# Kernel tuning notes

Hardware: AMD Instinct MI355X
Metric: run time of the kernel (lower is better)

## Reference

```python
import jax, jax.numpy as jnp
import numpy as np

T = 16384  # sequence length (scan axis)
D = 512    # d_model


def setup_inputs() -> dict:
    key = jax.random.key(0)
    k1, k2, k3, k4 = jax.random.split(key, 4)
    inputs = jax.random.normal(k1, (T, D), dtype=jnp.float32)
    terminations = jax.random.bernoulli(k2, 0.01, (T,))
    c0 = jnp.zeros((D,), dtype=jnp.float32)
    h0 = jnp.zeros((D,), dtype=jnp.float32)
    # flax OptimizedLSTMCell fuses the 4 gates (order i, f, g, o) into one kernel
    scale = 1.0 / np.sqrt(D).astype(np.float32)
    Wx = jax.random.normal(k3, (D, 4 * D), dtype=jnp.float32) * scale  # input kernel (no bias in flax)
    Wh = jax.random.normal(k4, (D, 4 * D), dtype=jnp.float32) * scale  # recurrent kernel
    b = jnp.zeros((4 * D,), dtype=jnp.float32)                          # recurrent-dense bias
    return {"inputs": inputs, "terminations": terminations, "c0": c0, "h0": h0,
            "Wx": Wx, "Wh": Wh, "b": b}


def reference(inputs, terminations, c0, h0, Wx, Wh, b):
    def step(carry, xt):
        x, term = xt
        c, h = carry
        # reset_on_terminate: zero the carry when this step begins a new episode
        keep = jnp.where(term, jnp.zeros((), c.dtype), jnp.ones((), c.dtype))
        c = c * keep
        h = h * keep
        # fused gate pre-activations, flax gate order: i, f, g, o
        z = x @ Wx + h @ Wh + b  # [4*D]
        i, f, g, o = jnp.split(z, 4, axis=-1)
        new_c = jax.nn.sigmoid(f) * c + jax.nn.sigmoid(i) * jnp.tanh(g)
        new_h = jax.nn.sigmoid(o) * jnp.tanh(new_c)
        return (new_c, new_h), (new_c, new_h)

    _, (cs, hs) = jax.lax.scan(step, (c0, h0), (inputs, terminations))
    # original returns (y_t, new_states) with y_t == new_h per step -> (hs, (cs, hs))
    return hs, cs, hs
```

## Files before the change

### kernel.cpp

```cpp
#include <hip/hip_runtime.h>

typedef _Float16 half8 __attribute__((ext_vector_type(8)));
typedef float floatx4 __attribute__((ext_vector_type(4)));
typedef unsigned int u32x4 __attribute__((ext_vector_type(4)));
typedef unsigned long long u64;
typedef unsigned int u32;
typedef unsigned short u16;

#define T_LEN 16384
#define DM 512
#define NC 2048
#define NG 16
#define NR 16
#define WPG 16
#define WVG 32

struct Meta { int S; int use_h0; int steps_g[NG]; };

union FragU { u64 q[2]; u32x4 r; half8 v; };

__device__ __forceinline__ float sigf(float x) { return 1.0f / (1.0f + __expf(-x)); }
__device__ __forceinline__ float tanh_f(float x) { return 1.0f - 2.0f / (__expf(2.0f * x) + 1.0f); }

__global__ void zero_kernel(u32* __restrict__ p, size_t nwords) {
    size_t i = (size_t)blockIdx.x * blockDim.x + threadIdx.x;
    size_t stride = (size_t)gridDim.x * blockDim.x;
    for (; i < nwords; i += stride) p[i] = 0u;
}

__global__ void pack_f16_kernel(const float* __restrict__ src, _Float16* __restrict__ dst, int n8) {
    int i = blockIdx.x * blockDim.x + threadIdx.x;
    if (i >= n8) return;
    const floatx4* s = (const floatx4*)src + (size_t)i * 2;
    floatx4 a = s[0], b = s[1];
    half8 o;
    o[0] = (_Float16)a[0]; o[1] = (_Float16)a[1]; o[2] = (_Float16)a[2]; o[3] = (_Float16)a[3];
    o[4] = (_Float16)b[0]; o[5] = (_Float16)b[1]; o[6] = (_Float16)b[2]; o[7] = (_Float16)b[3];
    ((half8*)dst)[i] = o;
}

__global__ __launch_bounds__(256) void pack_w_kernel(const float* __restrict__ src, half8* __restrict__ dst) {
    int wid = blockIdx.x * 4 + (threadIdx.x >> 6);
    int l = threadIdx.x & 63;
    int tt = wid >> 4, kt = wid & 15;
    int q = tt & 3, cch = tt >> 2;
    int col = q * 512 + cch * 16 + (l & 15);
    int h = l >> 4;
    half8 o;
#pragma unroll
    for (int jj = 0; jj < 8; jj++) o[jj] = (_Float16)src[(size_t)(kt * 32 + h * 8 + jj) * NC + col];
    dst[(tt * 16 + kt) * 64 + l] = o;
}

__global__ void prep_kernel(const void* __restrict__ termraw, const float* __restrict__ h0,
                            int* __restrict__ seg_start, int* __restrict__ seg_len,
                            Meta* __restrict__ meta, _Float16* __restrict__ Hbuf) {
    __shared__ int cnts[256], offs[256];
    __shared__ int nzm, oddnz, totS;
    __shared__ int chain[256];
    int tid = threadIdx.x;
    if (tid == 0) { nzm = 0; oddnz = 0; }
    __syncthreads();
    const unsigned char* tb = (const unsigned char*)termraw;
    const int* ti = (const int*)termraw;
    int lm = 0;
    for (int i = tid; i < T_LEN; i += 256) {
        if (tb[i]) {
            int p = i & 3;
            if (p == 1 || p == 2) lm |= 1;
            else if (p == 3) lm |= 2;
            else lm |= 4;
        }
    }
    if (lm) atomicOr(&nzm, lm);
    __syncthreads();
    int mm = nzm;
    int bytemode = (mm & 1) ? 1 : 0;
    int floatmode = (!bytemode && (mm & 2)) ? 1 : 0;
    int lo = 0;
    if (!bytemode && !floatmode) {
        for (int k2 = 2 * tid + 1; k2 < T_LEN; k2 += 512) if (ti[k2]) lo = 1;
    }
    if (lo) atomicOr(&oddnz, 1);
    __syncthreads();
    int i64mode = (!bytemode && !floatmode && oddnz == 0 && (mm & 4)) ? 1 : 0;
    const float* tf = (const float*)termraw;

    auto termAt = [&](int t) -> int {
        if (bytemode) return tb[t] != 0;
        if (floatmode) return tf[t] != 0.0f;
        if (i64mode) return (ti[2 * t] != 0) || (ti[2 * t + 1] != 0);
        return ti[t] != 0;
    };

    int base = tid * 64;
    int cnt = 0;
    for (int k = 0; k < 64; k++) {
        int t = base + k;
        if (t == 0 || termAt(t)) cnt++;
    }
    cnts[tid] = cnt;
    __syncthreads();
    if (tid == 0) {
        int a = 0;
        for (int i = 0; i < 256; i++) { offs[i] = a; a += cnts[i]; }
        totS = a;
        meta->S = a;
    }
    __syncthreads();
    int S = totS;
    {
        int o = offs[tid];
        for (int k = 0; k < 64; k++) {
            int t = base + k;
            if (t == 0 || termAt(t)) seg_start[o++] = t;
        }
    }
    __syncthreads();
    for (int i = tid; i < S; i += 256)
        seg_len[i] = ((i + 1 < S) ? seg_start[i + 1] : T_LEN) - seg_start[i];
    __syncthreads();
    {
        int g = tid >> 4, r = tid & 15;
        int tot = 0;
        for (int i = g + 16 * r; i < S; i += 256) tot += seg_len[i];
        chain[tid] = tot;
    }
    __syncthreads();
    if (tid < NG) {
        int mx = 0;
        for (int r = 0; r < 16; r++) mx = max(mx, chain[tid * 16 + r]);
        meta->steps_g[tid] = mx;
    }
    int u = termAt(0);
    if (tid == 0) meta->use_h0 = !u;
    if (!u) {
        for (int d2 = tid; d2 < DM; d2 += 256)
            Hbuf[(d2 >> 3) * 128 + (d2 & 7)] = (_Float16)h0[d2];
    }
}

__global__ __launch_bounds__(256) void xw_gemm_kernel(const half8* __restrict__ A, const half8* __restrict__ B,
                                                      const float* __restrict__ bias, _Float16* __restrict__ XW) {
    int bx = blockIdx.x, by = blockIdx.y;
    int w = threadIdx.x >> 6, l = threadIdx.x & 63;
    int mbase = bx * 64 + w * 16;
    int h = l >> 4, n = l & 15;
    floatx4 acc[8] = {};
    int arow = mbase + n;
#pragma unroll
    for (int kt = 0; kt < 16; kt++) {
        half8 a = A[(size_t)arow * 64 + kt * 4 + h];
#pragma unroll
        for (int nt = 0; nt < 8; nt++)
            acc[nt] = __builtin_amdgcn_mfma_f32_16x16x32_f16(a, B[((by * 8 + nt) * 16 + kt) * 64 + l], acc[nt], 0, 0, 0);
    }
#pragma unroll
    for (int nt = 0; nt < 8; nt++) {
        int tt = by * 8 + nt, q = tt & 3, cch = tt >> 2;
        float bv = bias[q * 512 + cch * 16 + n];
#pragma unroll
        for (int r = 0; r < 4; r++) {
            int row = mbase + h * 4 + r;
            XW[(size_t)row * NC + tt * 16 + n] = (_Float16)(acc[nt][r] + bv);
        }
    }
}

struct Trk { int seg, t0, s0, end, active; };

__device__ __forceinline__ void trk_init(Trk& k, int row, int g, int S,
                                         const int* __restrict__ ss, const int* __restrict__ sl) {
    int seg = g + 16 * row;
    k.seg = seg;
    if (seg < S) { k.t0 = ss[seg]; k.s0 = 0; k.end = sl[seg]; k.active = 1; }
    else { k.t0 = 0; k.s0 = 0; k.end = 0x7fffffff; k.active = 0; }
}

__device__ __forceinline__ int trk_step(Trk& k, int s, int S,
                                        const int* __restrict__ ss, const int* __restrict__ sl, int& t_out) {
    int z = !k.active;
    if (s > 0 && k.active && s == k.end) {
        int seg = k.seg + 256;
        if (seg < S) { k.seg = seg; k.t0 = ss[seg]; k.s0 = s; k.end = s + sl[seg]; z = 1; }
        else { k.active = 0; z = 1; }
    }
    t_out = k.active ? (k.t0 + (s - k.s0)) : 0;
    return z;
}

__global__ __launch_bounds__(192, 1) void scan_kernel(
    const half8* __restrict__ PW, const _Float16* __restrict__ XW,
    const float* __restrict__ c0,
    const int* __restrict__ seg_start, const int* __restrict__ seg_len,
    const Meta* __restrict__ meta,
    u64* __restrict__ Hbuf, int* __restrict__ flags,
    float* __restrict__ out) {
    const int b = blockIdx.x;
    const int g = (b & 7) * 2 + (b >> 7);
    const int jj = (b >> 3) & 15;
    const int tid = threadIdx.x;
    const int w = tid >> 6, l = tid & 63;
    const int S = meta->S;
    const int steps = meta->steps_g[g];
    if (steps <= 0) return;
    const int use_h0 = meta->use_h0;

    __shared__ __align__(16) u16 hstage[2][NR][16];
    __shared__ __align__(16) _Float16 xwstage[2][NR][128];
    __shared__ __align__(16) float outstage[2][2][NR][32];
    __shared__ int ioflag[2];
    __shared__ int outcnt[2];

    if (tid == 0) { ioflag[0] = -1; ioflag[1] = -1; outcnt[0] = 0; outcnt[1] = 0; }
    __syncthreads();

    float* outH = out;
    float* outC = out + (size_t)T_LEN * DM;
    float* outH2 = out + 2 * (size_t)T_LEN * DM;

    if (w < 2) {
        const int c = jj * 2 + w;
        const int n = l & 15, h = l >> 4;
        const int d = c * 16 + n;

        half8 bf[4][16];
#pragma unroll
        for (int q = 0; q < 4; q++)
#pragma unroll
            for (int kt = 0; kt < 16; kt++) {
                bf[q][kt] = PW[((c * 4 + q) * 16 + kt) * 64 + l];
                asm volatile("" : "+v"(bf[q][kt]));
            }

        Trk trkM; trk_init(trkM, n, g, S, seg_start, seg_len);
        Trk trk[4];
#pragma unroll
        for (int r = 0; r < 4; r++) trk_init(trk[r], h * 4 + r, g, S, seg_start, seg_len);

        float cc[4];
#pragma unroll
        for (int r = 0; r < 4; r++) {
            int row = h * 4 + r;
            cc[r] = (g == 0 && row == 0 && use_h0) ? c0[d] : 0.0f;
        }

        FragU zu; zu.q[0] = 0; zu.q[1] = 0;
        const half8 zfrag = zu.v;

        int* fl = flags + g * WVG;
        const int wfid = jj * 2 + w;
        const int pollidx = l & 31;

        const int b2 = l >> 5, m2 = (l >> 1) & 15, half = l & 1;
        const int ktc = c >> 1, hhp = (c & 1) * 2 + b2;
        const int ldsIdx = m2 * 4 + b2 * 2 + half;
        const size_t hwIdx = (size_t)(ktc * 4 + hhp) * 32 + m2 * 2 + half;

        for (int s = 0; s < steps; ++s) {
            int tdump;
            const int zM = trk_step(trkM, s, S, seg_start, seg_len, tdump);
            int zz[4];
#pragma unroll
            for (int r = 0; r < 4; r++)
                zz[r] = trk_step(trk[r], s, S, seg_start, seg_len, tdump);

            while (__hip_atomic_load(&ioflag[s & 1], __ATOMIC_RELAXED, __HIP_MEMORY_SCOPE_WORKGROUP) < s)
                __builtin_amdgcn_s_sleep(1);
            asm volatile("" ::: "memory");
            float xwv[4][4];
#pragma unroll
            for (int q = 0; q < 4; q++)
#pragma unroll
                for (int r = 0; r < 4; r++)
                    xwv[q][r] = (float)xwstage[s & 1][h * 4 + r][w * 64 + q * 16 + n];

            if (s > 0) {
                while (true) {
                    int v = __hip_atomic_load(&fl[pollidx], __ATOMIC_RELAXED, __HIP_MEMORY_SCOPE_AGENT);
                    if (__all(v >= s)) break;
                    __builtin_amdgcn_s_sleep(1);
                }
                asm volatile("" ::: "memory");
            }

            const int rp = s & 1;
            u64* Hr = Hbuf + (size_t)(g * 2 + rp) * (NR * DM / 4);
            u64* Hw = Hbuf + (size_t)(g * 2 + (rp ^ 1)) * (NR * DM / 4);

            const int m = n;
            u32x4 raw[16];
#pragma unroll
            for (int kt = 0; kt < 16; kt++) {
                const void* ap = (const char*)Hr + (((size_t)kt * 64 + h * 16 + m) << 4);
                asm volatile("global_load_dwordx4 %0, %1, off sc1" : "=v"(raw[kt]) : "v"(ap) : "memory");
            }
            asm volatile("s_waitcnt vmcnt(0)" ::: "memory");
            __builtin_amdgcn_sched_barrier(0);
            half8 afr[16];
#pragma unroll
            for (int kt = 0; kt < 16; kt++) {
                FragU u; u.r = raw[kt];
                afr[kt] = zM ? zfrag : u.v;
            }

            floatx4 acc[4] = {};
#pragma unroll
            for (int kt = 0; kt < 16; kt++) {
#pragma unroll
                for (int q = 0; q < 4; q++)
                    acc[q] = __builtin_amdgcn_mfma_f32_16x16x32_f16(afr[kt], bf[q][kt], acc[q], 0, 0, 0);
            }

            float hnv[4], cnv[4];
#pragma unroll
            for (int r = 0; r < 4; r++) {
                float zi = acc[0][r] + xwv[0][r];
                float zf = acc[1][r] + xwv[1][r];
                float zg = acc[2][r] + xwv[2][r];
                float zo = acc[3][r] + xwv[3][r];
                float cprev = zz[r] ? 0.0f : cc[r];
                float cn = sigf(zf) * cprev + sigf(zi) * tanh_f(zg);
                float hn = sigf(zo) * tanh_f(cn);
                cc[r] = cn; hnv[r] = hn; cnv[r] = cn;
                hstage[w][h * 4 + r][n] = __builtin_bit_cast(u16, (_Float16)hn);
            }

            asm volatile("s_waitcnt lgkmcnt(0)" ::: "memory");
            __builtin_amdgcn_sched_barrier(0);
            u64 pk = ((const u64*)&hstage[w][0][0])[ldsIdx];
            __hip_atomic_store(&Hw[hwIdx], pk, __ATOMIC_RELAXED, __HIP_MEMORY_SCOPE_AGENT);

            asm volatile("s_waitcnt vmcnt(0)" ::: "memory");
            if (l == 0)
                __hip_atomic_store(&fl[wfid], s + 1, __ATOMIC_RELAXED, __HIP_MEMORY_SCOPE_AGENT);

            while (__hip_atomic_load(&outcnt[s & 1], __ATOMIC_RELAXED, __HIP_MEMORY_SCOPE_WORKGROUP) == 2)
                __builtin_amdgcn_s_sleep(1);
            asm volatile("" ::: "memory");
#pragma unroll
            for (int r = 0; r < 4; r++) {
                outstage[s & 1][0][h * 4 + r][w * 16 + n] = hnv[r];
                outstage[s & 1][1][h * 4 + r][w * 16 + n] = cnv[r];
            }
            asm volatile("s_waitcnt lgkmcnt(0)" ::: "memory");
            if (l == 0)
                __hip_atomic_fetch_add(&outcnt[s & 1], 1, __ATOMIC_RELAXED, __HIP_MEMORY_SCOPE_WORKGROUP);
        }
    } else {
        const int rX = l >> 4;
        const int rO = l >> 3;
        Trk trkX[4];
#pragma unroll
        for (int i = 0; i < 4; i++) trk_init(trkX[i], rX + 4 * i, g, S, seg_start, seg_len);
        Trk trkO[2];
        trk_init(trkO[0], rO, g, S, seg_start, seg_len);
        trk_init(trkO[1], rO + 8, g, S, seg_start, seg_len);

        auto stageXW = [&](int step, int buf) {
            int tX[4], td;
#pragma unroll
            for (int i = 0; i < 4; i++) (void)trk_step(trkX[i], step, S, seg_start, seg_len, tX[i]);
            u32x4 xr[4];
#pragma unroll
            for (int i = 0; i < 4; i++)
                xr[i] = *(const u32x4*)((const char*)XW + ((size_t)tX[i] * NC + jj * 128 + (l & 15) * 8) * 2);
            (void)td;
#pragma unroll
            for (int i = 0; i < 4; i++)
                *(u32x4*)&xwstage[buf][rX + 4 * i][(l & 15) * 8] = xr[i];
            asm volatile("s_waitcnt lgkmcnt(0)" ::: "memory");
            if (l == 0)
                __hip_atomic_store(&ioflag[buf], step, __ATOMIC_RELAXED, __HIP_MEMORY_SCOPE_WORKGROUP);
        };

        stageXW(0, 0);
        stageXW(1, 1);

        for (int s = 0; s < steps; ++s) {
            int tO[2], aO[2];
#pragma unroll
            for (int j2 = 0; j2 < 2; j2++) {
                (void)trk_step(trkO[j2], s, S, seg_start, seg_len, tO[j2]);
                aO[j2] = trkO[j2].active;
            }
            while (__hip_atomic_load(&outcnt[s & 1], __ATOMIC_RELAXED, __HIP_MEMORY_SCOPE_WORKGROUP) < 2)
                __builtin_amdgcn_s_sleep(1);
            asm volatile("" ::: "memory");
            floatx4 hv[2], cv[2];
#pragma unroll
            for (int j2 = 0; j2 < 2; j2++) {
                hv[j2] = *(floatx4*)&outstage[s & 1][0][rO + 8 * j2][(l & 7) * 4];
                cv[j2] = *(floatx4*)&outstage[s & 1][1][rO + 8 * j2][(l & 7) * 4];
            }
            asm volatile("s_waitcnt lgkmcnt(0)" ::: "memory");
            __hip_atomic_store(&outcnt[s & 1], 0, __ATOMIC_RELAXED, __HIP_MEMORY_SCOPE_WORKGROUP);
#pragma unroll
            for (int j2 = 0; j2 < 2; j2++) {
                if (aO[j2]) {
                    size_t base = (size_t)tO[j2] * DM + jj * 32 + (l & 7) * 4;
                    *(floatx4*)&outH[base] = hv[j2];
                    *(floatx4*)&outC[base] = cv[j2];
                    *(floatx4*)&outH2[base] = hv[j2];
                }
            }
            stageXW(s + 2, s & 1);
        }
    }
}

extern "C" void kernel_launch(void* const* d_in, const int* in_sizes, int n_in,
                              void* d_out, int out_size, void* d_ws, size_t ws_size,
                              hipStream_t stream) {
    const float* inputs = (const float*)d_in[0];
    const void* terms = d_in[1];
    const float* c0 = (const float*)d_in[2];
    const float* h0 = (const float*)d_in[3];
    const float* Wx = (const float*)d_in[4];
    const float* Wh = (const float*)d_in[5];
    const float* bias = (const float*)d_in[6];
    float* out = (float*)d_out;

    size_t off = 0;
    auto take = [&](size_t bts) { size_t cur = off; off = (off + bts + 255) & ~(size_t)255; return cur; };
    size_t offXW = take((size_t)T_LEN * NC * 2);
    size_t offAin = take((size_t)T_LEN * DM * 2);
    size_t offPX = take((size_t)DM * NC * 2);
    size_t offPW = take((size_t)DM * NC * 2);
    size_t offSS = take((size_t)(T_LEN + 2) * 4);
    size_t offSL = take((size_t)(T_LEN + 2) * 4);
    size_t offH = take(2ull * NG * NR * DM * 2);
    size_t offFL = take((size_t)NG * WVG * 4);
    size_t offME = take(256);
    size_t total = off;
    (void)ws_size;

    char* W = (char*)d_ws;
    _Float16* Ain = (_Float16*)(W + offAin);
    half8* PX = (half8*)(W + offPX);
    half8* PWp = (half8*)(W + offPW);
    int* segS = (int*)(W + offSS);
    int* segL = (int*)(W + offSL);
    Meta* meta = (Meta*)(W + offME);
    _Float16* XWp = (_Float16*)(W + offXW);

    size_t zwords = (total - offH) / 4;
    zero_kernel<<<256, 256, 0, stream>>>((u32*)(W + offH), zwords);
    pack_f16_kernel<<<(T_LEN * DM / 8 + 255) / 256, 256, 0, stream>>>(inputs, Ain, T_LEN * DM / 8);
    pack_w_kernel<<<512, 256, 0, stream>>>(Wx, PX);
    pack_w_kernel<<<512, 256, 0, stream>>>(Wh, PWp);
    prep_kernel<<<1, 256, 0, stream>>>(terms, h0, segS, segL, meta, (_Float16*)(W + offH));

    dim3 gg(T_LEN / 64, NC / 128);
    xw_gemm_kernel<<<gg, 256, 0, stream>>>((const half8*)Ain, (const half8*)PX, bias, XWp);
    scan_kernel<<<256, 192, 0, stream>>>((const half8*)PWp, XWp, c0, segS, segL, meta,
                                         (u64*)(W + offH), (int*)(W + offFL), out);
}
```

Measured before the change: 1.799 ms.

## Replace per-step flag barrier with tagged hidden-state words and LDS-resident weights

Removes the separate global flag array and its store-then-poll handshake. Each 32-bit hidden-state payload is now stored next to a step tag in an 8-byte word, so consumers spin on the data loads themselves until every tag matches the current step. This drops one round trip of global-memory latency from the critical path of every recurrent step. It also moves half of the recurrent weight fragments from registers into LDS to ease register pressure. In exchange the hidden-state buffer doubles in size, each step issues four times as many narrower loads, and the correctness now relies on 8-byte stores being observed atomically.

```diff
diff --git a/kernel.cpp b/kernel.cpp
--- a/kernel.cpp
+++ b/kernel.cpp
@@ -3,6 +3,7 @@
 typedef _Float16 half8 __attribute__((ext_vector_type(8)));
 typedef float floatx4 __attribute__((ext_vector_type(4)));
 typedef unsigned int u32x4 __attribute__((ext_vector_type(4)));
+typedef unsigned int u32x2 __attribute__((ext_vector_type(2)));
 typedef unsigned long long u64;
 typedef unsigned int u32;
 typedef unsigned short u16;
@@ -13,7 +14,7 @@
 #define NG 16
 #define NR 16
 #define WPG 16
-#define WVG 32
+#define HBYTES (4096 * 8)
 
 struct Meta { int S; int use_h0; int steps_g[NG]; };
 
@@ -135,8 +136,11 @@
     int u = termAt(0);
     if (tid == 0) meta->use_h0 = !u;
     if (!u) {
-        for (int d2 = tid; d2 < DM; d2 += 256)
-            Hbuf[(d2 >> 3) * 128 + (d2 & 7)] = (_Float16)h0[d2];
+        for (int d2 = tid; d2 < DM; d2 += 256) {
+            int v8chunk = ((d2 >> 5) * 64 + ((d2 >> 3) & 3) * 16) * 2 + ((d2 >> 2) & 1);
+            int c8 = v8chunk * 2 + ((d2 >> 1) & 1);
+            Hbuf[c8 * 4 + (d2 & 1)] = (_Float16)h0[d2];
+        }
     }
 }
 
@@ -194,8 +198,7 @@
     const float* __restrict__ c0,
     const int* __restrict__ seg_start, const int* __restrict__ seg_len,
     const Meta* __restrict__ meta,
-    u64* __restrict__ Hbuf, int* __restrict__ flags,
-    float* __restrict__ out) {
+    char* __restrict__ Hbuf, float* __restrict__ out) {
     const int b = blockIdx.x;
     const int g = (b & 7) * 2 + (b >> 7);
     const int jj = (b >> 3) & 15;
@@ -209,10 +212,19 @@
     __shared__ __align__(16) u16 hstage[2][NR][16];
     __shared__ __align__(16) _Float16 xwstage[2][NR][128];
     __shared__ __align__(16) float outstage[2][2][NR][32];
+    __shared__ __align__(16) half8 whlds[2][2][16][64];
     __shared__ int ioflag[2];
     __shared__ int outcnt[2];
 
     if (tid == 0) { ioflag[0] = -1; ioflag[1] = -1; outcnt[0] = 0; outcnt[1] = 0; }
+    if (w < 2) {
+        const int c0i = jj * 2 + w;
+#pragma unroll
+        for (int kt = 0; kt < 16; kt++)
+#pragma unroll
+            for (int qq = 0; qq < 2; qq++)
+                whlds[w][qq][kt][l] = PW[((c0i * 4 + 2 + qq) * 16 + kt) * 64 + l];
+    }
     __syncthreads();
 
     float* outH = out;
@@ -223,14 +235,15 @@
         const int c = jj * 2 + w;
         const int n = l & 15, h = l >> 4;
         const int d = c * 16 + n;
-
-        half8 bf[4][16];
-#pragma unroll
-        for (int q = 0; q < 4; q++)
+        const int m = n;
+
+        half8 bfv[2][16];
+#pragma unroll
+        for (int q = 0; q < 2; q++)
 #pragma unroll
             for (int kt = 0; kt < 16; kt++) {
-                bf[q][kt] = PW[((c * 4 + q) * 16 + kt) * 64 + l];
-                asm volatile("" : "+v"(bf[q][kt]));
+                bfv[q][kt] = PW[((c * 4 + q) * 16 + kt) * 64 + l];
+                asm volatile("" : "+v"(bfv[q][kt]));
             }
 
         Trk trkM; trk_init(trkM, n, g, S, seg_start, seg_len);
@@ -248,14 +261,10 @@
         FragU zu; zu.q[0] = 0; zu.q[1] = 0;
         const half8 zfrag = zu.v;
 
-        int* fl = flags + g * WVG;
-        const int wfid = jj * 2 + w;
-        const int pollidx = l & 31;
-
         const int b2 = l >> 5, m2 = (l >> 1) & 15, half = l & 1;
         const int ktc = c >> 1, hhp = (c & 1) * 2 + b2;
         const int ldsIdx = m2 * 4 + b2 * 2 + half;
-        const size_t hwIdx = (size_t)(ktc * 4 + hhp) * 32 + m2 * 2 + half;
+        const int v8chunk = (ktc * 4 + hhp) * 32 + m2 * 2 + half;
 
         for (int s = 0; s < steps; ++s) {
             int tdump;
@@ -275,41 +284,46 @@
                 for (int r = 0; r < 4; r++)
                     xwv[q][r] = (float)xwstage[s & 1][h * 4 + r][w * 64 + q * 16 + n];
 
-            if (s > 0) {
-                while (true) {
-                    int v = __hip_atomic_load(&fl[pollidx], __ATOMIC_RELAXED, __HIP_MEMORY_SCOPE_AGENT);
-                    if (__all(v >= s)) break;
-                    __builtin_amdgcn_s_sleep(1);
+            const char* Hrb = Hbuf + (size_t)(g * 2 + (s & 1)) * HBYTES;
+            const char* p0 = Hrb + ((h * 16 + m) << 5);
+            u32x2 raw[64];
+            while (true) {
+#pragma unroll
+                for (int kt = 0; kt < 16; kt++) {
+                    const char* ap = p0 + (kt << 11);
+                    asm volatile("global_load_dwordx2 %0, %1, off sc1" : "=v"(raw[4 * kt]) : "v"(ap) : "memory");
+                    asm volatile("global_load_dwordx2 %0, %1, off offset:8 sc1" : "=v"(raw[4 * kt + 1]) : "v"(ap) : "memory");
+                    asm volatile("global_load_dwordx2 %0, %1, off offset:16 sc1" : "=v"(raw[4 * kt + 2]) : "v"(ap) : "memory");
+                    asm volatile("global_load_dwordx2 %0, %1, off offset:24 sc1" : "=v"(raw[4 * kt + 3]) : "v"(ap) : "memory");
                 }
-                asm volatile("" ::: "memory");
-            }
-
-            const int rp = s & 1;
-            u64* Hr = Hbuf + (size_t)(g * 2 + rp) * (NR * DM / 4);
-            u64* Hw = Hbuf + (size_t)(g * 2 + (rp ^ 1)) * (NR * DM / 4);
-
-            const int m = n;
-            u32x4 raw[16];
+                asm volatile("s_waitcnt vmcnt(0)" ::: "memory");
+                __builtin_amdgcn_sched_barrier(0);
+                u32 bad = 0;
+#pragma unroll
+                for (int kt = 0; kt < 16; kt++)
+                    bad |= (raw[4 * kt][1] ^ (u32)s) | (raw[4 * kt + 1][1] ^ (u32)s)
+                         | (raw[4 * kt + 2][1] ^ (u32)s) | (raw[4 * kt + 3][1] ^ (u32)s);
+                if (__all(bad == 0)) break;
+                __builtin_amdgcn_s_sleep(1);
+            }
+            half8 afr[16];
 #pragma unroll
             for (int kt = 0; kt < 16; kt++) {
-                const void* ap = (const char*)Hr + (((size_t)kt * 64 + h * 16 + m) << 4);
-                asm volatile("global_load_dwordx4 %0, %1, off sc1" : "=v"(raw[kt]) : "v"(ap) : "memory");
-            }
-            asm volatile("s_waitcnt vmcnt(0)" ::: "memory");
-            __builtin_amdgcn_sched_barrier(0);
-            half8 afr[16];
+                FragU u;
+                u.r[0] = raw[4 * kt][0];
+                u.r[1] = raw[4 * kt + 1][0];
+                u.r[2] = raw[4 * kt + 2][0];
+                u.r[3] = raw[4 * kt + 3][0];
+                afr[kt] = zM ? zfrag : u.v;
+            }
+
+            floatx4 acc[4] = {};
 #pragma unroll
             for (int kt = 0; kt < 16; kt++) {
-                FragU u; u.r = raw[kt];
-                afr[kt] = zM ? zfrag : u.v;
-            }
-
-            floatx4 acc[4] = {};
-#pragma unroll
-            for (int kt = 0; kt < 16; kt++) {
-#pragma unroll
-                for (int q = 0; q < 4; q++)
-                    acc[q] = __builtin_amdgcn_mfma_f32_16x16x32_f16(afr[kt], bf[q][kt], acc[q], 0, 0, 0);
+                acc[0] = __builtin_amdgcn_mfma_f32_16x16x32_f16(afr[kt], bfv[0][kt], acc[0], 0, 0, 0);
+                acc[1] = __builtin_amdgcn_mfma_f32_16x16x32_f16(afr[kt], bfv[1][kt], acc[1], 0, 0, 0);
+                acc[2] = __builtin_amdgcn_mfma_f32_16x16x32_f16(afr[kt], whlds[w][0][kt][l], acc[2], 0, 0, 0);
+                acc[3] = __builtin_amdgcn_mfma_f32_16x16x32_f16(afr[kt], whlds[w][1][kt][l], acc[3], 0, 0, 0);
             }
 
             float hnv[4], cnv[4];
@@ -329,11 +343,15 @@
             asm volatile("s_waitcnt lgkmcnt(0)" ::: "memory");
             __builtin_amdgcn_sched_barrier(0);
             u64 pk = ((const u64*)&hstage[w][0][0])[ldsIdx];
-            __hip_atomic_store(&Hw[hwIdx], pk, __ATOMIC_RELAXED, __HIP_MEMORY_SCOPE_AGENT);
-
-            asm volatile("s_waitcnt vmcnt(0)" ::: "memory");
-            if (l == 0)
-                __hip_atomic_store(&fl[wfid], s + 1, __ATOMIC_RELAXED, __HIP_MEMORY_SCOPE_AGENT);
+
+            char* Hwb = Hbuf + (size_t)(g * 2 + ((s & 1) ^ 1)) * HBYTES;
+            u32 tag = (u32)(s + 1);
+            u32x2 stA, stB;
+            stA[0] = (u32)pk;         stA[1] = tag;
+            stB[0] = (u32)(pk >> 32); stB[1] = tag;
+            char* hwp = Hwb + ((size_t)v8chunk << 4);
+            asm volatile("global_store_dwordx2 %0, %1, off sc1" :: "v"(hwp), "v"(stA) : "memory");
+            asm volatile("global_store_dwordx2 %0, %1, off offset:8 sc1" :: "v"(hwp), "v"(stB) : "memory");
 
             while (__hip_atomic_load(&outcnt[s & 1], __ATOMIC_RELAXED, __HIP_MEMORY_SCOPE_WORKGROUP) == 2)
                 __builtin_amdgcn_s_sleep(1);
@@ -358,14 +376,13 @@
         trk_init(trkO[1], rO + 8, g, S, seg_start, seg_len);
 
         auto stageXW = [&](int step, int buf) {
-            int tX[4], td;
+            int tX[4];
 #pragma unroll
             for (int i = 0; i < 4; i++) (void)trk_step(trkX[i], step, S, seg_start, seg_len, tX[i]);
             u32x4 xr[4];
 #pragma unroll
             for (int i = 0; i < 4; i++)
                 xr[i] = *(const u32x4*)((const char*)XW + ((size_t)tX[i] * NC + jj * 128 + (l & 15) * 8) * 2);
-            (void)td;
 #pragma unroll
             for (int i = 0; i < 4; i++)
                 *(u32x4*)&xwstage[buf][rX + 4 * i][(l & 15) * 8] = xr[i];
@@ -429,8 +446,7 @@
     size_t offPW = take((size_t)DM * NC * 2);
     size_t offSS = take((size_t)(T_LEN + 2) * 4);
     size_t offSL = take((size_t)(T_LEN + 2) * 4);
-    size_t offH = take(2ull * NG * NR * DM * 2);
-    size_t offFL = take((size_t)NG * WVG * 4);
+    size_t offH = take(2ull * NG * HBYTES);
     size_t offME = take(256);
     size_t total = off;
     (void)ws_size;
@@ -454,5 +470,5 @@
     dim3 gg(T_LEN / 64, NC / 128);
     xw_gemm_kernel<<<gg, 256, 0, stream>>>((const half8*)Ain, (const half8*)PX, bias, XWp);
     scan_kernel<<<256, 192, 0, stream>>>((const half8*)PWp, XWp, c0, segS, segL, meta,
-                                         (u64*)(W + offH), (int*)(W + offFL), out);
-}
+                                         (char*)(W + offH), out);
+}
```

Result: slower. 3.760 ms (+109.0%).

## Probe L2 coherence at runtime and use sc0 cached path for cross-block handoff

Applied to the files above, without the earlier changes.

Adds a startup probe in which the 16 blocks of each group exchange tokens through sc0 (non-bypassing) loads and stores, and all agree on whether they see each other's writes. If every probe round succeeds, the recurrent loop uses sc0 loads and stores for the hidden-state buffer and progress flags instead of sc1 loads and agent-scope atomics. The aim is lower latency for the per-step cross-block exchange by keeping it in a shared cache level. The risk is relying on an empirical coherence check: if the blocks of a group do not actually share that cache, stale data could be read, and the probe itself adds startup spinning.

```diff
diff --git a/kernel.cpp b/kernel.cpp
--- a/kernel.cpp
+++ b/kernel.cpp
@@ -14,6 +14,8 @@
 #define NR 16
 #define WPG 16
 #define WVG 32
+#define PROBE_ROUNDS 12
+#define PROBE_CAP 4000
 
 struct Meta { int S; int use_h0; int steps_g[NG]; };
 
@@ -189,12 +191,178 @@
     return z;
 }
 
+template <bool L2C>
+__device__ __forceinline__ void run_compute(
+    const half8* __restrict__ PW, const _Float16* __restrict__ XW,
+    const float* __restrict__ c0,
+    const int* __restrict__ seg_start, const int* __restrict__ seg_len,
+    u64* __restrict__ Hbuf, int* __restrict__ flags,
+    int g, int jj, int w, int l, int steps, int S, int use_h0,
+    u16 (&hstage)[2][NR][16], _Float16 (&xwstage)[2][NR][128],
+    float (&outstage)[2][2][NR][32], int (&ioflag)[2], int (&outcnt)[2]) {
+    const int c = jj * 2 + w;
+    const int n = l & 15, h = l >> 4;
+    const int d = c * 16 + n;
+    const int m = n;
+
+    half8 bf[4][16];
+#pragma unroll
+    for (int q = 0; q < 4; q++)
+#pragma unroll
+        for (int kt = 0; kt < 16; kt++) {
+            bf[q][kt] = PW[((c * 4 + q) * 16 + kt) * 64 + l];
+            asm volatile("" : "+v"(bf[q][kt]));
+        }
+
+    Trk trkM; trk_init(trkM, n, g, S, seg_start, seg_len);
+    Trk trk[4];
+#pragma unroll
+    for (int r = 0; r < 4; r++) trk_init(trk[r], h * 4 + r, g, S, seg_start, seg_len);
+
+    float cc[4];
+#pragma unroll
+    for (int r = 0; r < 4; r++) {
+        int row = h * 4 + r;
+        cc[r] = (g == 0 && row == 0 && use_h0) ? c0[d] : 0.0f;
+    }
+
+    FragU zu; zu.q[0] = 0; zu.q[1] = 0;
+    const half8 zfrag = zu.v;
+
+    int* fl = flags + g * WVG;
+    const int wfid = jj * 2 + w;
+    const int pollidx = l & 31;
+
+    const int b2 = l >> 5, m2 = (l >> 1) & 15, half = l & 1;
+    const int ktc = c >> 1, hhp = (c & 1) * 2 + b2;
+    const int ldsIdx = m2 * 4 + b2 * 2 + half;
+    const size_t hwIdx = (size_t)(ktc * 4 + hhp) * 32 + m2 * 2 + half;
+
+    for (int s = 0; s < steps; ++s) {
+        int tdump;
+        const int zM = trk_step(trkM, s, S, seg_start, seg_len, tdump);
+        int zz[4];
+#pragma unroll
+        for (int r = 0; r < 4; r++)
+            zz[r] = trk_step(trk[r], s, S, seg_start, seg_len, tdump);
+
+        while (__hip_atomic_load(&ioflag[s & 1], __ATOMIC_RELAXED, __HIP_MEMORY_SCOPE_WORKGROUP) < s)
+            __builtin_amdgcn_s_sleep(1);
+        asm volatile("" ::: "memory");
+        float xwv[4][4];
+#pragma unroll
+        for (int q = 0; q < 4; q++)
+#pragma unroll
+            for (int r = 0; r < 4; r++)
+                xwv[q][r] = (float)xwstage[s & 1][h * 4 + r][w * 64 + q * 16 + n];
+
+        if (s > 0) {
+            if constexpr (L2C) {
+                const int* flp = &fl[pollidx];
+                while (true) {
+                    int v;
+                    asm volatile("global_load_dword %0, %1, off sc0" : "=v"(v) : "v"(flp) : "memory");
+                    asm volatile("s_waitcnt vmcnt(0)" ::: "memory");
+                    if (__all(v >= s)) break;
+                    __builtin_amdgcn_s_sleep(1);
+                }
+                asm volatile("" ::: "memory");
+            } else {
+                while (true) {
+                    int v = __hip_atomic_load(&fl[pollidx], __ATOMIC_RELAXED, __HIP_MEMORY_SCOPE_AGENT);
+                    if (__all(v >= s)) break;
+                    __builtin_amdgcn_s_sleep(1);
+                }
+                asm volatile("" ::: "memory");
+            }
+        }
+
+        const int rp = s & 1;
+        u64* Hr = Hbuf + (size_t)(g * 2 + rp) * (NR * DM / 4);
+        u64* Hw = Hbuf + (size_t)(g * 2 + (rp ^ 1)) * (NR * DM / 4);
+
+        u32x4 raw[16];
+#pragma unroll
+        for (int kt = 0; kt < 16; kt++) {
+            const void* ap = (const char*)Hr + (((size_t)kt * 64 + h * 16 + m) << 4);
+            if constexpr (L2C)
+                asm volatile("global_load_dwordx4 %0, %1, off sc0" : "=v"(raw[kt]) : "v"(ap) : "memory");
+            else
+                asm volatile("global_load_dwordx4 %0, %1, off sc1" : "=v"(raw[kt]) : "v"(ap) : "memory");
+        }
+        asm volatile("s_waitcnt vmcnt(0)" ::: "memory");
+        __builtin_amdgcn_sched_barrier(0);
+        half8 afr[16];
+#pragma unroll
+        for (int kt = 0; kt < 16; kt++) {
+            FragU u; u.r = raw[kt];
+            afr[kt] = zM ? zfrag : u.v;
+        }
+
+        floatx4 acc[4] = {};
+#pragma unroll
+        for (int kt = 0; kt < 16; kt++) {
+#pragma unroll
+            for (int q = 0; q < 4; q++)
+                acc[q] = __builtin_amdgcn_mfma_f32_16x16x32_f16(afr[kt], bf[q][kt], acc[q], 0, 0, 0);
+        }
+
+        float hnv[4], cnv[4];
+#pragma unroll
+        for (int r = 0; r < 4; r++) {
+            float zi = acc[0][r] + xwv[0][r];
+            float zf = acc[1][r] + xwv[1][r];
+            float zg = acc[2][r] + xwv[2][r];
+            float zo = acc[3][r] + xwv[3][r];
+            float cprev = zz[r] ? 0.0f : cc[r];
+            float cn = sigf(zf) * cprev + sigf(zi) * tanh_f(zg);
+            float hn = sigf(zo) * tanh_f(cn);
+            cc[r] = cn; hnv[r] = hn; cnv[r] = cn;
+            hstage[w][h * 4 + r][n] = __builtin_bit_cast(u16, (_Float16)hn);
+        }
+
+        asm volatile("s_waitcnt lgkmcnt(0)" ::: "memory");
+        __builtin_amdgcn_sched_barrier(0);
+        u64 pk = ((const u64*)&hstage[w][0][0])[ldsIdx];
+        if constexpr (L2C) {
+            u64* hwp = &Hw[hwIdx];
+            asm volatile("global_store_dwordx2 %0, %1, off sc0" :: "v"(hwp), "v"(pk) : "memory");
+        } else {
+            __hip_atomic_store(&Hw[hwIdx], pk, __ATOMIC_RELAXED, __HIP_MEMORY_SCOPE_AGENT);
+        }
+
+        asm volatile("s_waitcnt vmcnt(0)" ::: "memory");
+        if (l == 0) {
+            int sp1 = s + 1;
+            if constexpr (L2C) {
+                int* flw = &fl[wfid];
+                asm volatile("global_store_dword %0, %1, off sc0" :: "v"(flw), "v"(sp1) : "memory");
+            } else {
+                __hip_atomic_store(&fl[wfid], sp1, __ATOMIC_RELAXED, __HIP_MEMORY_SCOPE_AGENT);
+            }
+        }
+
+        while (__hip_atomic_load(&outcnt[s & 1], __ATOMIC_RELAXED, __HIP_MEMORY_SCOPE_WORKGROUP) == 2)
+            __builtin_amdgcn_s_sleep(1);
+        asm volatile("" ::: "memory");
+#pragma unroll
+        for (int r = 0; r < 4; r++) {
+            outstage[s & 1][0][h * 4 + r][w * 16 + n] = hnv[r];
+            outstage[s & 1][1][h * 4 + r][w * 16 + n] = cnv[r];
+        }
+        asm volatile("s_waitcnt lgkmcnt(0)" ::: "memory");
+        if (l == 0)
+            __hip_atomic_fetch_add(&outcnt[s & 1], 1, __ATOMIC_RELAXED, __HIP_MEMORY_SCOPE_WORKGROUP);
+    }
+}
+
 __global__ __launch_bounds__(192, 1) void scan_kernel(
     const half8* __restrict__ PW, const _Float16* __restrict__ XW,
     const float* __restrict__ c0,
     const int* __restrict__ seg_start, const int* __restrict__ seg_len,
     const Meta* __restrict__ meta,
     u64* __restrict__ Hbuf, int* __restrict__ flags,
+    u32* __restrict__ probebuf, int* __restrict__ verdict,
     float* __restrict__ out) {
     const int b = blockIdx.x;
     const int g = (b & 7) * 2 + (b >> 7);
@@ -211,142 +379,58 @@
     __shared__ __align__(16) float outstage[2][2][NR][32];
     __shared__ int ioflag[2];
     __shared__ int outcnt[2];
+    __shared__ int sh_l2ok;
 
     if (tid == 0) { ioflag[0] = -1; ioflag[1] = -1; outcnt[0] = 0; outcnt[1] = 0; }
-    __syncthreads();
+
+    if (w == 0) {
+        int okflag = 1;
+        u32* pb = probebuf + g * 64;
+        for (int r = 0; r < PROBE_ROUNDS && okflag; ++r) {
+            u32 tok = 0x10000u | ((u32)r << 8) | (u32)jj;
+            if (l == 0) {
+                u32* tp = pb + jj;
+                asm volatile("global_store_dword %0, %1, off sc0" :: "v"(tp), "v"(tok) : "memory");
+                asm volatile("s_waitcnt vmcnt(0)" ::: "memory");
+            }
+            u32 want = 0x10000u | ((u32)r << 8) | (u32)(l & 15);
+            const u32* mp = pb + (l & 15);
+            int got = 0;
+            for (int it = 0; it < PROBE_CAP; ++it) {
+                u32 tv;
+                asm volatile("global_load_dword %0, %1, off sc0" : "=v"(tv) : "v"(mp) : "memory");
+                asm volatile("s_waitcnt vmcnt(0)" ::: "memory");
+                if (__all(tv >= want)) { got = 1; break; }
+                __builtin_amdgcn_s_sleep(1);
+            }
+            if (!got) okflag = 0;
+        }
+        if (l == 0)
+            __hip_atomic_store(&verdict[g * 16 + jj], okflag ? 2 : 1, __ATOMIC_RELAXED, __HIP_MEMORY_SCOPE_AGENT);
+        int vv;
+        while (true) {
+            vv = __hip_atomic_load(&verdict[g * 16 + (l & 15)], __ATOMIC_RELAXED, __HIP_MEMORY_SCOPE_AGENT);
+            if (__all(vv != 0)) break;
+            __builtin_amdgcn_s_sleep(1);
+        }
+        if (l == 0) sh_l2ok = __all(vv == 2) ? 1 : 0;
+    }
+    __syncthreads();
+    const int l2ok = sh_l2ok;
 
     float* outH = out;
     float* outC = out + (size_t)T_LEN * DM;
     float* outH2 = out + 2 * (size_t)T_LEN * DM;
 
     if (w < 2) {
-        const int c = jj * 2 + w;
-        const int n = l & 15, h = l >> 4;
-        const int d = c * 16 + n;
-
-        half8 bf[4][16];
-#pragma unroll
-        for (int q = 0; q < 4; q++)
-#pragma unroll
-            for (int kt = 0; kt < 16; kt++) {
-                bf[q][kt] = PW[((c * 4 + q) * 16 + kt) * 64 + l];
-                asm volatile("" : "+v"(bf[q][kt]));
-            }
-
-        Trk trkM; trk_init(trkM, n, g, S, seg_start, seg_len);
-        Trk trk[4];
-#pragma unroll
-        for (int r = 0; r < 4; r++) trk_init(trk[r], h * 4 + r, g, S, seg_start, seg_len);
-
-        float cc[4];
-#pragma unroll
-        for (int r = 0; r < 4; r++) {
-            int row = h * 4 + r;
-            cc[r] = (g == 0 && row == 0 && use_h0) ? c0[d] : 0.0f;
-        }
-
-        FragU zu; zu.q[0] = 0; zu.q[1] = 0;
-        const half8 zfrag = zu.v;
-
-        int* fl = flags + g * WVG;
-        const int wfid = jj * 2 + w;
-        const int pollidx = l & 31;
-
-        const int b2 = l >> 5, m2 = (l >> 1) & 15, half = l & 1;
-        const int ktc = c >> 1, hhp = (c & 1) * 2 + b2;
-        const int ldsIdx = m2 * 4 + b2 * 2 + half;
-        const size_t hwIdx = (size_t)(ktc * 4 + hhp) * 32 + m2 * 2 + half;
-
-        for (int s = 0; s < steps; ++s) {
-            int tdump;
-            const int zM = trk_step(trkM, s, S, seg_start, seg_len, tdump);
-            int zz[4];
-#pragma unroll
-            for (int r = 0; r < 4; r++)
-                zz[r] = trk_step(trk[r], s, S, seg_start, seg_len, tdump);
-
-            while (__hip_atomic_load(&ioflag[s & 1], __ATOMIC_RELAXED, __HIP_MEMORY_SCOPE_WORKGROUP) < s)
-                __builtin_amdgcn_s_sleep(1);
-            asm volatile("" ::: "memory");
-            float xwv[4][4];
-#pragma unroll
-            for (int q = 0; q < 4; q++)
-#pragma unroll
-                for (int r = 0; r < 4; r++)
-                    xwv[q][r] = (float)xwstage[s & 1][h * 4 + r][w * 64 + q * 16 + n];
-
-            if (s > 0) {
-                while (true) {
-                    int v = __hip_atomic_load(&fl[pollidx], __ATOMIC_RELAXED, __HIP_MEMORY_SCOPE_AGENT);
-                    if (__all(v >= s)) break;
-                    __builtin_amdgcn_s_sleep(1);
-                }
-                asm volatile("" ::: "memory");
-            }
-
-            const int rp = s & 1;
-            u64* Hr = Hbuf + (size_t)(g * 2 + rp) * (NR * DM / 4);
-            u64* Hw = Hbuf + (size_t)(g * 2 + (rp ^ 1)) * (NR * DM / 4);
-
-            const int m = n;
-            u32x4 raw[16];
-#pragma unroll
-            for (int kt = 0; kt < 16; kt++) {
-                const void* ap = (const char*)Hr + (((size_t)kt * 64 + h * 16 + m) << 4);
-                asm volatile("global_load_dwordx4 %0, %1, off sc1" : "=v"(raw[kt]) : "v"(ap) : "memory");
-            }
-            asm volatile("s_waitcnt vmcnt(0)" ::: "memory");
-            __builtin_amdgcn_sched_barrier(0);
-            half8 afr[16];
-#pragma unroll
-            for (int kt = 0; kt < 16; kt++) {
-                FragU u; u.r = raw[kt];
-                afr[kt] = zM ? zfrag : u.v;
-            }
-
-            floatx4 acc[4] = {};
-#pragma unroll
-            for (int kt = 0; kt < 16; kt++) {
-#pragma unroll
-                for (int q = 0; q < 4; q++)
-                    acc[q] = __builtin_amdgcn_mfma_f32_16x16x32_f16(afr[kt], bf[q][kt], acc[q], 0, 0, 0);
-            }
-
-            float hnv[4], cnv[4];
-#pragma unroll
-            for (int r = 0; r < 4; r++) {
-                float zi = acc[0][r] + xwv[0][r];
-                float zf = acc[1][r] + xwv[1][r];
-                float zg = acc[2][r] + xwv[2][r];
-                float zo = acc[3][r] + xwv[3][r];
-                float cprev = zz[r] ? 0.0f : cc[r];
-                float cn = sigf(zf) * cprev + sigf(zi) * tanh_f(zg);
-                float hn = sigf(zo) * tanh_f(cn);
-                cc[r] = cn; hnv[r] = hn; cnv[r] = cn;
-                hstage[w][h * 4 + r][n] = __builtin_bit_cast(u16, (_Float16)hn);
-            }
-
-            asm volatile("s_waitcnt lgkmcnt(0)" ::: "memory");
-            __builtin_amdgcn_sched_barrier(0);
-            u64 pk = ((const u64*)&hstage[w][0][0])[ldsIdx];
-            __hip_atomic_store(&Hw[hwIdx], pk, __ATOMIC_RELAXED, __HIP_MEMORY_SCOPE_AGENT);
-
-            asm volatile("s_waitcnt vmcnt(0)" ::: "memory");
-            if (l == 0)
-                __hip_atomic_store(&fl[wfid], s + 1, __ATOMIC_RELAXED, __HIP_MEMORY_SCOPE_AGENT);
-
-            while (__hip_atomic_load(&outcnt[s & 1], __ATOMIC_RELAXED, __HIP_MEMORY_SCOPE_WORKGROUP) == 2)
-                __builtin_amdgcn_s_sleep(1);
-            asm volatile("" ::: "memory");
-#pragma unroll
-            for (int r = 0; r < 4; r++) {
-                outstage[s & 1][0][h * 4 + r][w * 16 + n] = hnv[r];
-                outstage[s & 1][1][h * 4 + r][w * 16 + n] = cnv[r];
-            }
-            asm volatile("s_waitcnt lgkmcnt(0)" ::: "memory");
-            if (l == 0)
-                __hip_atomic_fetch_add(&outcnt[s & 1], 1, __ATOMIC_RELAXED, __HIP_MEMORY_SCOPE_WORKGROUP);
-        }
+        if (l2ok)
+            run_compute<true>(PW, XW, c0, seg_start, seg_len, Hbuf, flags,
+                              g, jj, w, l, steps, S, use_h0,
+                              hstage, xwstage, outstage, ioflag, outcnt);
+        else
+            run_compute<false>(PW, XW, c0, seg_start, seg_len, Hbuf, flags,
+                               g, jj, w, l, steps, S, use_h0,
+                               hstage, xwstage, outstage, ioflag, outcnt);
     } else {
         const int rX = l >> 4;
         const int rO = l >> 3;
@@ -358,14 +442,13 @@
         trk_init(trkO[1], rO + 8, g, S, seg_start, seg_len);
 
         auto stageXW = [&](int step, int buf) {
-            int tX[4], td;
+            int tX[4];
 #pragma unroll
             for (int i = 0; i < 4; i++) (void)trk_step(trkX[i], step, S, seg_start, seg_len, tX[i]);
             u32x4 xr[4];
 #pragma unroll
             for (int i = 0; i < 4; i++)
                 xr[i] = *(const u32x4*)((const char*)XW + ((size_t)tX[i] * NC + jj * 128 + (l & 15) * 8) * 2);
-            (void)td;
 #pragma unroll
             for (int i = 0; i < 4; i++)
                 *(u32x4*)&xwstage[buf][rX + 4 * i][(l & 15) * 8] = xr[i];
@@ -431,6 +514,8 @@
     size_t offSL = take((size_t)(T_LEN + 2) * 4);
     size_t offH = take(2ull * NG * NR * DM * 2);
     size_t offFL = take((size_t)NG * WVG * 4);
+    size_t offPB = take((size_t)NG * 256);
+    size_t offVD = take((size_t)NG * WPG * 4);
     size_t offME = take(256);
     size_t total = off;
     (void)ws_size;
@@ -454,5 +539,6 @@
     dim3 gg(T_LEN / 64, NC / 128);
     xw_gemm_kernel<<<gg, 256, 0, stream>>>((const half8*)Ain, (const half8*)PX, bias, XWp);
     scan_kernel<<<256, 192, 0, stream>>>((const half8*)PWp, XWp, c0, segS, segL, meta,
-                                         (u64*)(W + offH), (int*)(W + offFL), out);
-}
+                                         (u64*)(W + offH), (int*)(W + offFL),
+                                         (u32*)(W + offPB), (int*)(W + offVD), out);
+}
```

After: 2.215 ms. 23.2% more time.
